# Kernel tuning notes

Measured on AMD Instinct MI355X. Metric: run time of the kernel, lower is better.

## Reference

```python
import jax, jax.numpy as jnp
import numpy as np

HID = 768        # config.hidden_size
MM_HID = 1024    # config.mmodal_hidden_size
N_Q = 64         # config.num_queries
WIN = 512        # config.window_size
LN_EPS = 1e-5


def _window_starts(m, n, w):
    # mirrors split_tensor's start-index logic (static, computed in numpy)
    step = max(1, (m - w) // (n - 1))
    starts = []
    for i in range(n):
        s = i * step
        if s + w > m:
            s = m - w
        starts.append(s)
    return np.asarray(starts, dtype=np.int32)


def layernorm(x, g, b):
    mu = jnp.mean(x, axis=-1, keepdims=True)
    var = jnp.var(x, axis=-1, keepdims=True)
    return (x - mu) * jax.lax.rsqrt(var + LN_EPS) * g + b


def setup_inputs() -> dict:
    key = jax.random.key(0)
    ks = jax.random.split(key, 12)
    b, m, li = 4, 8192, 77
    s = lambda fan_in: 1.0 / np.sqrt(fan_in)
    inp = {
        'x_mmodal': jax.random.normal(ks[0], (b, m, MM_HID), jnp.float32),
        'inst_feats': jax.random.normal(ks[1], (b, li, HID), jnp.float32),
        'queries': jax.random.normal(ks[2], (1, N_Q, HID), jnp.float32),
        'W_proj': jax.random.normal(ks[3], (HID, HID), jnp.float32) * s(HID),
        'b_proj': jnp.zeros((HID,), jnp.float32),
        'W_kv_inst': jax.random.normal(ks[4], (HID, 2 * HID), jnp.float32) * s(HID),
        'b_kv_inst': jnp.zeros((2 * HID,), jnp.float32),
        'W_out_inst': jax.random.normal(ks[5], (HID, HID), jnp.float32) * s(HID),
        'b_out_inst': jnp.zeros((HID,), jnp.float32),
        'W_kv_mm': jax.random.normal(ks[6], (MM_HID, 2 * HID), jnp.float32) * s(MM_HID),
        'b_kv_mm': jnp.zeros((2 * HID,), jnp.float32),
        'W_out_mm': jax.random.normal(ks[7], (HID, HID), jnp.float32) * s(HID),
        'b_out_mm': jnp.zeros((HID,), jnp.float32),
        'ln_g': jnp.ones((HID,), jnp.float32),
        'ln_b': jnp.zeros((HID,), jnp.float32),
    }
    return inp


def reference(x_mmodal, inst_feats, queries, W_proj, b_proj, W_kv_inst,
              b_kv_inst, W_out_inst, b_out_inst, W_kv_mm, b_kv_mm,
              W_out_mm, b_out_mm, ln_g, ln_b):
    b = x_mmodal.shape[0]
    scale = 1.0 / jnp.sqrt(jnp.asarray(HID, x_mmodal.dtype))

    # ---- dense cross-attention over instruction features ----
    inst = inst_feats @ W_proj + b_proj                      # (b, li, d)
    k, v = jnp.split(inst @ W_kv_inst + b_kv_inst, 2, axis=-1)
    k = layernorm(k, ln_g, ln_b)
    v = layernorm(v, ln_g, ln_b)
    q = jnp.broadcast_to(queries, (b, N_Q, HID))
    attn = jnp.einsum('bnd,bmd->bnm', q, k) * scale
    attn = jax.nn.softmax(attn, axis=-1)
    q = jnp.einsum('bnm,bmd->bnd', attn, v)
    q = layernorm(q @ W_out_inst + b_out_inst, ln_g, ln_b)

    # ---- swin-style overlapping windowed cross-attention over mmodal ----
    k, v = jnp.split(x_mmodal @ W_kv_mm + b_kv_mm, 2, axis=-1)
    k = layernorm(k, ln_g, ln_b)
    v = layernorm(v, ln_g, ln_b)
    m = k.shape[1]
    starts = _window_starts(m, N_Q, WIN)                     # (n,)
    idx = jnp.asarray(starts[:, None] + np.arange(WIN))      # (n, w)
    kw = k[:, idx]                                           # (b, n, w, d)
    vw = v[:, idx]                                           # (b, n, w, d)
    a = jnp.einsum('bnd,bnwd->bnw', q, kw) * scale
    a = jax.nn.softmax(a, axis=-1)
    out = jnp.einsum('bnw,bnwd->bnd', a, vw)
    out = layernorm(out @ W_out_mm + b_out_mm, ln_g, ln_b)
    return out
```

## Files before the change

### kernel.cpp

```cpp
#include <hip/hip_runtime.h>

#define HIDDEN 768
#define NQ 64
#define WINSZ 512
#define MSEQ 8192
#define BATCH 4
#define LI 77
#define MMHID 1024
#define LN_EPS 1e-5f
#define SCALE_QK 0.03608439182435161f

typedef __attribute__((ext_vector_type(8))) short short8v;
typedef __attribute__((ext_vector_type(4))) float f32x4;
typedef __attribute__((ext_vector_type(8))) unsigned short u16x8;

#define AS1 __attribute__((address_space(1)))
#define AS3 __attribute__((address_space(3)))

__device__ inline unsigned short f2bf(float f) {
    unsigned u = __float_as_uint(f);
    u += 0x7fffu + ((u >> 16) & 1u);
    return (unsigned short)(u >> 16);
}
__device__ inline float bf2f(unsigned short h) {
    return __uint_as_float(((unsigned)h) << 16);
}

__device__ inline void block_reduce2_256(float& s1, float& s2, float* sm) {
    #pragma unroll
    for (int o = 32; o; o >>= 1) { s1 += __shfl_down(s1, o); s2 += __shfl_down(s2, o); }
    int lane = threadIdx.x & 63, w = threadIdx.x >> 6;
    __syncthreads();
    if (lane == 0) { sm[w] = s1; sm[4 + w] = s2; }
    __syncthreads();
    s1 = sm[0] + sm[1] + sm[2] + sm[3];
    s2 = sm[4] + sm[5] + sm[6] + sm[7];
}

__global__ __launch_bounds__(256) void cvt_kernel(const float* __restrict__ in,
                                                  unsigned short* __restrict__ out, int n8) {
    int i = blockIdx.x * 256 + threadIdx.x;
    if (i >= n8) return;
    const float4* p = (const float4*)(in + (size_t)i * 8);
    float4 a = p[0], b = p[1];
    u16x8 o;
    o[0] = f2bf(a.x); o[1] = f2bf(a.y); o[2] = f2bf(a.z); o[3] = f2bf(a.w);
    o[4] = f2bf(b.x); o[5] = f2bf(b.y); o[6] = f2bf(b.z); o[7] = f2bf(b.w);
    *(u16x8*)(out + (size_t)i * 8) = o;
}

__global__ __launch_bounds__(256) void cvt_pad_kernel(const float* __restrict__ in,
                                                      unsigned short* __restrict__ out,
                                                      int n8_valid, int n8_total) {
    int i = blockIdx.x * 256 + threadIdx.x;
    if (i >= n8_total) return;
    u16x8 o = {};
    if (i < n8_valid) {
        const float4* p = (const float4*)(in + (size_t)i * 8);
        float4 a = p[0], b = p[1];
        o[0] = f2bf(a.x); o[1] = f2bf(a.y); o[2] = f2bf(a.z); o[3] = f2bf(a.w);
        o[4] = f2bf(b.x); o[5] = f2bf(b.y); o[6] = f2bf(b.z); o[7] = f2bf(b.w);
    }
    *(u16x8*)(out + (size_t)i * 8) = o;
}

__global__ __launch_bounds__(256) void cvt_q_kernel(const float* __restrict__ q2,
                                                    const float* __restrict__ g,
                                                    unsigned short* __restrict__ q2bf,
                                                    float* __restrict__ qgsum) {
    int blk = blockIdx.x;
    int b = blk >> 7, r = blk & 127;
    int t = threadIdx.x;
    unsigned short* orow = q2bf + (size_t)blk * HIDDEN;
    if (r >= 64) {
        orow[t] = 0; orow[t + 256] = 0; orow[t + 512] = 0;
        return;
    }
    const float* qrow = q2 + ((size_t)(b * 64 + r)) * HIDDEN;
    float v0 = qrow[t]       * g[t]       * SCALE_QK;
    float v1 = qrow[t + 256] * g[t + 256] * SCALE_QK;
    float v2 = qrow[t + 512] * g[t + 512] * SCALE_QK;
    orow[t] = f2bf(v0); orow[t + 256] = f2bf(v1); orow[t + 512] = f2bf(v2);
    float s = v0 + v1 + v2, s2 = 0.f;
    __shared__ float sm[8];
    block_reduce2_256(s, s2, sm);
    if (t == 0) qgsum[b * 64 + r] = s;
}

struct TWJobs {
    const float* W[5];
    unsigned short* Wt[5];
    int D[5];
    int C[5];
};
__global__ __launch_bounds__(256) void transW_all_kernel(TWJobs tw) {
    int z = blockIdx.z;
    int C = tw.C[z], D = tw.D[z];
    int n0 = blockIdx.x * 32, k0 = blockIdx.y * 32;
    if (n0 >= C || k0 >= D) return;
    const float* W = tw.W[z];
    unsigned short* Wt = tw.Wt[z];
    __shared__ float tile[32][33];
    int tx = threadIdx.x & 31, ty = (threadIdx.x >> 5);
    #pragma unroll
    for (int i = 0; i < 32; i += 8)
        tile[ty + i][tx] = W[(size_t)(k0 + ty + i) * C + n0 + tx];
    __syncthreads();
    #pragma unroll
    for (int i = 0; i < 32; i += 8)
        Wt[(size_t)(n0 + ty + i) * D + k0 + tx] = f2bf(tile[tx][ty + i]);
}

#define GM 32768
#define GN 1536
#define GK 1024

__global__ __launch_bounds__(256) void gemm_kv_kernel(const unsigned short* __restrict__ A,
                                                      const unsigned short* __restrict__ Bt,
                                                      const float* __restrict__ bias,
                                                      unsigned short* __restrict__ C) {
    __shared__ unsigned short sA[128 * 64];
    __shared__ unsigned short sB[128 * 64];

    int nwg = gridDim.x;
    int bid = blockIdx.x;
    int wg = bid;
    if ((nwg & 7) == 0) { int cpx = nwg >> 3; wg = (bid & 7) * cpx + (bid >> 3); }
    int bm = wg / (GN / 128), bn = wg % (GN / 128);
    int row0 = bm * 128, col0 = bn * 128;

    int tid = threadIdx.x;
    int lane = tid & 63, wid = tid >> 6;
    int wr = wid >> 1, wc = wid & 1;

    f32x4 acc[4][4] = {};

    int rS[4], cS[4];
    #pragma unroll
    for (int i = 0; i < 4; i++) {
        int ch = wid * 4 + i;
        int r = ch * 8 + (lane >> 3);
        rS[i] = r;
        cS[i] = ((lane & 7) ^ (r & 7)) << 3;
    }

    for (int k0 = 0; k0 < GK; k0 += 64) {
        #pragma unroll
        for (int i = 0; i < 4; i++) {
            int ch = wid * 4 + i;
            const unsigned short* ga = A + (size_t)(row0 + rS[i]) * GK + k0 + cS[i];
            __builtin_amdgcn_global_load_lds((const AS1 unsigned int*)ga,
                                             (AS3 unsigned int*)&sA[ch * 512], 16, 0, 0);
            const unsigned short* gb = Bt + (size_t)(col0 + rS[i]) * GK + k0 + cS[i];
            __builtin_amdgcn_global_load_lds((const AS1 unsigned int*)gb,
                                             (AS3 unsigned int*)&sB[ch * 512], 16, 0, 0);
        }
        __syncthreads();

        #pragma unroll
        for (int kk = 0; kk < 64; kk += 32) {
            int ko = (kk + ((lane >> 4) << 3)) * 2;
            short8v af[4], bf[4];
            #pragma unroll
            for (int m = 0; m < 4; m++) {
                int r = wr * 64 + m * 16 + (lane & 15);
                int addr = r * 128 + (ko ^ ((r & 7) << 4));
                af[m] = *(const short8v*)((const char*)sA + addr);
            }
            #pragma unroll
            for (int n = 0; n < 4; n++) {
                int r = wc * 64 + n * 16 + (lane & 15);
                int addr = r * 128 + (ko ^ ((r & 7) << 4));
                bf[n] = *(const short8v*)((const char*)sB + addr);
            }
            #pragma unroll
            for (int m = 0; m < 4; m++)
                #pragma unroll
                for (int n = 0; n < 4; n++)
                    acc[m][n] = __builtin_amdgcn_mfma_f32_16x16x32_bf16(af[m], bf[n], acc[m][n], 0, 0, 0);
        }
        __syncthreads();
    }

    int crow = (lane >> 4) * 4;
    int ccol = lane & 15;
    #pragma unroll
    for (int m = 0; m < 4; m++) {
        #pragma unroll
        for (int n = 0; n < 4; n++) {
            int gc = col0 + wc * 64 + n * 16 + ccol;
            float bv = bias[gc];
            #pragma unroll
            for (int j = 0; j < 4; j++) {
                int gr = row0 + wr * 64 + m * 16 + crow + j;
                C[(size_t)gr * GN + gc] = f2bf(acc[m][n][j] + bv);
            }
        }
    }
}

__global__ __launch_bounds__(256) void stats_kernel(const unsigned short* __restrict__ kv,
                                                    float2* __restrict__ stats) {
    int rh = blockIdx.x;
    const unsigned short* p = kv + (size_t)rh * 768;
    int t = threadIdx.x;
    float x0 = bf2f(p[t]), x1 = bf2f(p[t + 256]), x2 = bf2f(p[t + 512]);
    float s = x0 + x1 + x2, s2 = x0 * x0 + x1 * x1 + x2 * x2;
    __shared__ float sm[8];
    block_reduce2_256(s, s2, sm);
    if (t == 0) {
        float mu = s * (1.f / 768.f);
        float var = s2 * (1.f / 768.f) - mu * mu;
        float inv = rsqrtf(var + LN_EPS);
        stats[rh] = make_float2(mu * inv, inv);
    }
}

template <int TK, bool OUT_BF16>
__global__ __launch_bounds__(256) void gemm_tile_kernel(const unsigned short* __restrict__ A,
                                                        const unsigned short* __restrict__ Bt,
                                                        const float* __restrict__ bias,
                                                        void* __restrict__ Cout, int N) {
    __shared__ unsigned short sA[128 * 64];
    __shared__ unsigned short sB[128 * 64];

    int row0 = blockIdx.x * 128, col0 = blockIdx.y * 128;
    int tid = threadIdx.x;
    int lane = tid & 63, wid = tid >> 6;
    int wr = wid >> 1, wc = wid & 1;

    f32x4 acc[4][4] = {};

    int rS[4], cS[4];
    #pragma unroll
    for (int i = 0; i < 4; i++) {
        int ch = wid * 4 + i;
        int r = ch * 8 + (lane >> 3);
        rS[i] = r;
        cS[i] = ((lane & 7) ^ (r & 7)) << 3;
    }

    for (int k0 = 0; k0 < TK; k0 += 64) {
        #pragma unroll
        for (int i = 0; i < 4; i++) {
            int ch = wid * 4 + i;
            const unsigned short* ga = A + (size_t)(row0 + rS[i]) * TK + k0 + cS[i];
            __builtin_amdgcn_global_load_lds((const AS1 unsigned int*)ga,
                                             (AS3 unsigned int*)&sA[ch * 512], 16, 0, 0);
            const unsigned short* gb = Bt + (size_t)(col0 + rS[i]) * TK + k0 + cS[i];
            __builtin_amdgcn_global_load_lds((const AS1 unsigned int*)gb,
                                             (AS3 unsigned int*)&sB[ch * 512], 16, 0, 0);
        }
        __syncthreads();

        #pragma unroll
        for (int kk = 0; kk < 64; kk += 32) {
            int ko = (kk + ((lane >> 4) << 3)) * 2;
            short8v af[4], bf[4];
            #pragma unroll
            for (int m = 0; m < 4; m++) {
                int r = wr * 64 + m * 16 + (lane & 15);
                int addr = r * 128 + (ko ^ ((r & 7) << 4));
                af[m] = *(const short8v*)((const char*)sA + addr);
            }
            #pragma unroll
            for (int n = 0; n < 4; n++) {
                int r = wc * 64 + n * 16 + (lane & 15);
                int addr = r * 128 + (ko ^ ((r & 7) << 4));
                bf[n] = *(const short8v*)((const char*)sB + addr);
            }
            #pragma unroll
            for (int m = 0; m < 4; m++)
                #pragma unroll
                for (int n = 0; n < 4; n++)
                    acc[m][n] = __builtin_amdgcn_mfma_f32_16x16x32_bf16(af[m], bf[n], acc[m][n], 0, 0, 0);
        }
        __syncthreads();
    }

    int crow = (lane >> 4) * 4;
    int ccol = lane & 15;
    #pragma unroll
    for (int m = 0; m < 4; m++) {
        #pragma unroll
        for (int n = 0; n < 4; n++) {
            int gc = col0 + wc * 64 + n * 16 + ccol;
            float bv = bias[gc];
            #pragma unroll
            for (int j = 0; j < 4; j++) {
                int gr = row0 + wr * 64 + m * 16 + crow + j;
                float v = acc[m][n][j] + bv;
                if (OUT_BF16) ((unsigned short*)Cout)[(size_t)gr * N + gc] = f2bf(v);
                else          ((float*)Cout)[(size_t)gr * N + gc] = v;
            }
        }
    }
}

__global__ __launch_bounds__(256) void gemm_scores_kernel(const unsigned short* __restrict__ Aall,
                                                          const unsigned short* __restrict__ kv,
                                                          float* __restrict__ scores) {
    __shared__ unsigned short sA[128 * 64];
    __shared__ unsigned short sB[128 * 64];

    int b = blockIdx.y;
    int col0 = blockIdx.x * 128;
    const unsigned short* A = Aall + (size_t)b * 128 * HIDDEN;
    const unsigned short* Bt = kv + (size_t)b * MSEQ * 1536;

    int tid = threadIdx.x;
    int lane = tid & 63, wid = tid >> 6;
    int wr = wid >> 1, wc = wid & 1;

    f32x4 acc[4][4] = {};

    int rS[4], cS[4];
    #pragma unroll
    for (int i = 0; i < 4; i++) {
        int ch = wid * 4 + i;
        int r = ch * 8 + (lane >> 3);
        rS[i] = r;
        cS[i] = ((lane & 7) ^ (r & 7)) << 3;
    }

    for (int k0 = 0; k0 < HIDDEN; k0 += 64) {
        #pragma unroll
        for (int i = 0; i < 4; i++) {
            int ch = wid * 4 + i;
            const unsigned short* ga = A + (size_t)rS[i] * HIDDEN + k0 + cS[i];
            __builtin_amdgcn_global_load_lds((const AS1 unsigned int*)ga,
                                             (AS3 unsigned int*)&sA[ch * 512], 16, 0, 0);
            const unsigned short* gb = Bt + (size_t)(col0 + rS[i]) * 1536 + k0 + cS[i];
            __builtin_amdgcn_global_load_lds((const AS1 unsigned int*)gb,
                                             (AS3 unsigned int*)&sB[ch * 512], 16, 0, 0);
        }
        __syncthreads();

        #pragma unroll
        for (int kk = 0; kk < 64; kk += 32) {
            int ko = (kk + ((lane >> 4) << 3)) * 2;
            short8v af[4], bf[4];
            #pragma unroll
            for (int m = 0; m < 4; m++) {
                int r = wr * 64 + m * 16 + (lane & 15);
                int addr = r * 128 + (ko ^ ((r & 7) << 4));
                af[m] = *(const short8v*)((const char*)sA + addr);
            }
            #pragma unroll
            for (int n = 0; n < 4; n++) {
                int r = wc * 64 + n * 16 + (lane & 15);
                int addr = r * 128 + (ko ^ ((r & 7) << 4));
                bf[n] = *(const short8v*)((const char*)sB + addr);
            }
            #pragma unroll
            for (int m = 0; m < 4; m++)
                #pragma unroll
                for (int n = 0; n < 4; n++)
                    acc[m][n] = __builtin_amdgcn_mfma_f32_16x16x32_bf16(af[m], bf[n], acc[m][n], 0, 0, 0);
        }
        __syncthreads();
    }

    int crow = (lane >> 4) * 4;
    int ccol = lane & 15;
    #pragma unroll
    for (int m = 0; m < 4; m++) {
        #pragma unroll
        for (int n = 0; n < 4; n++) {
            int gc = col0 + wc * 64 + n * 16 + ccol;
            #pragma unroll
            for (int j = 0; j < 4; j++) {
                int gr = wr * 64 + m * 16 + crow + j;
                if (gr < 64)
                    scores[((size_t)(b * 64 + gr)) * MSEQ + gc] = acc[m][n][j];
            }
        }
    }
}

__global__ __launch_bounds__(512) void win_softmax_kernel(const float* __restrict__ scores,
                                                          const float2* __restrict__ stats,
                                                          const float* __restrict__ qgsum,
                                                          unsigned short* __restrict__ P_abs,
                                                          float* __restrict__ s2out) {
    int bidx = blockIdx.x;
    int b = bidx >> 6, n = bidx & 63;
    int step = (MSEQ - WINSZ) / (NQ - 1);
    int s = n * step;
    if (s + WINSZ > MSEQ) s = MSEQ - WINSZ;

    __shared__ float sm[8];
    int t = threadIdx.x, lane = t & 63, w = t >> 6;
    int r_abs = s + t;
    size_t rowidx = (size_t)b * MSEQ + r_abs;
    float2 stk = stats[rowidx * 2 + 0];
    float qg = qgsum[b * 64 + n];
    float a = stk.y * scores[((size_t)(b * 64 + n)) * MSEQ + r_abs] - qg * stk.x;

    float m = a;
    #pragma unroll
    for (int o = 32; o; o >>= 1) m = fmaxf(m, __shfl_down(m, o));
    if (lane == 0) sm[w] = m;
    __syncthreads();
    m = sm[0];
    #pragma unroll
    for (int i = 1; i < 8; i++) m = fmaxf(m, sm[i]);
    float e = expf(a - m);
    float ssum = e;
    #pragma unroll
    for (int o = 32; o; o >>= 1) ssum += __shfl_down(ssum, o);
    __syncthreads();
    if (lane == 0) sm[w] = ssum;
    __syncthreads();
    ssum = 0;
    #pragma unroll
    for (int i = 0; i < 8; i++) ssum += sm[i];
    float p = e / ssum;

    float2 stv = stats[rowidx * 2 + 1];
    float pt = p * stv.y;
    float s2p = p * stv.x;
    #pragma unroll
    for (int o = 32; o; o >>= 1) s2p += __shfl_down(s2p, o);
    __syncthreads();
    if (lane == 0) sm[w] = s2p;
    __syncthreads();
    if (t == 0) {
        float s2 = 0;
        #pragma unroll
        for (int i = 0; i < 8; i++) s2 += sm[i];
        s2out[b * 64 + n] = s2;
    }

    unsigned short* prow = P_abs + ((size_t)(b * 64 + n)) * MSEQ;
    for (int pos = t; pos < MSEQ; pos += 512)
        if (pos < s || pos >= s + WINSZ) prow[pos] = 0;
    prow[r_abs] = f2bf(pt);
}

__global__ __launch_bounds__(768) void pv_chunk_kernel(const unsigned short* __restrict__ P_abs,
                                                       const unsigned short* __restrict__ kv,
                                                       float* __restrict__ out_acc) {
    int b = blockIdx.y;
    int r0 = blockIdx.x * 64;
    int t = threadIdx.x;

    int n_lo = (r0 >= 512) ? ((r0 - 512) / 121 + 1) : 0;
    int n_hi = (r0 + 63) / 121;
    if (n_hi > 63) n_hi = 63;

    __shared__ float pw[5][64];
    if (t < 5 * 64) {
        int ni = t >> 6, r = t & 63;
        int n = n_lo + ni;
        float v = 0.f;
        if (n <= n_hi)
            v = bf2f(P_abs[((size_t)(b * 64 + n)) * MSEQ + r0 + r]);
        pw[ni][r] = v;
    }
    __syncthreads();

    const unsigned short* vbase = kv + ((size_t)(b * MSEQ + r0)) * 1536 + 768;
    float acc[5] = {};
    #pragma unroll 8
    for (int r = 0; r < 64; ++r) {
        float v = bf2f(vbase[(size_t)r * 1536 + t]);
        #pragma unroll
        for (int ni = 0; ni < 5; ni++) acc[ni] = fmaf(v, pw[ni][r], acc[ni]);
    }
    #pragma unroll
    for (int ni = 0; ni < 5; ni++) {
        int n = n_lo + ni;
        if (n <= n_hi)
            atomicAdd(&out_acc[((size_t)(b * 64 + n)) * HIDDEN + t], acc[ni]);
    }
}

__global__ __launch_bounds__(256) void out_affine_kernel(const float* __restrict__ o_acc,
                                                         const float* __restrict__ s2,
                                                         const float* __restrict__ g,
                                                         const float* __restrict__ bb,
                                                         unsigned short* __restrict__ a_bf) {
    int i = blockIdx.x * 256 + threadIdx.x;
    if (i >= BATCH * NQ * HIDDEN) return;
    int n = i / HIDDEN, d = i - n * HIDDEN;
    a_bf[i] = f2bf(g[d] * (o_acc[i] - s2[n]) + bb[d]);
}

__global__ __launch_bounds__(256) void ln_f32_rows(float* __restrict__ base,
                                                   const float* __restrict__ g,
                                                   const float* __restrict__ b) {
    int rh = blockIdx.x;
    float* p = base + (size_t)rh * 768;
    int t = threadIdx.x;
    float x0 = p[t], x1 = p[t + 256], x2 = p[t + 512];
    float s = x0 + x1 + x2, s2 = x0 * x0 + x1 * x1 + x2 * x2;
    __shared__ float sm[8];
    block_reduce2_256(s, s2, sm);
    float mu = s * (1.f / 768.f);
    float var = s2 * (1.f / 768.f) - mu * mu;
    float inv = rsqrtf(var + LN_EPS);
    p[t]       = (x0 - mu) * inv * g[t]       + b[t];
    p[t + 256] = (x1 - mu) * inv * g[t + 256] + b[t + 256];
    p[t + 512] = (x2 - mu) * inv * g[t + 512] + b[t + 512];
}

__global__ __launch_bounds__(256) void attn_inst_kernel(const float* __restrict__ queries,
                                                        const float* __restrict__ kv,
                                                        unsigned short* __restrict__ qatt) {
    int bidx = blockIdx.x;
    int b = bidx >> 6, n = bidx & 63;
    __shared__ float qs[HIDDEN];
    __shared__ float sc[LI], sc2[LI];
    int t = threadIdx.x, lane = t & 63, w = t >> 6;
    const float* q = queries + (size_t)n * HIDDEN;
    for (int d = t; d < HIDDEN; d += 256) qs[d] = q[d];
    __syncthreads();
    const float* kb = kv + (size_t)b * LI * 1536;
    for (int j = w; j < LI; j += 4) {
        const float* kr = kb + (size_t)j * 1536;
        float a = 0;
        #pragma unroll
        for (int i = 0; i < 12; i++) { int d = lane + i * 64; a = fmaf(kr[d], qs[d], a); }
        #pragma unroll
        for (int o = 32; o; o >>= 1) a += __shfl_down(a, o);
        if (lane == 0) sc[j] = a * SCALE_QK;
    }
    __syncthreads();
    float m = -1e30f;
    for (int j = 0; j < LI; j++) m = fmaxf(m, sc[j]);
    if (t < LI) sc2[t] = expf(sc[t] - m);
    __syncthreads();
    float s = 0;
    for (int j = 0; j < LI; j++) s += sc2[j];
    float inv = 1.f / s;
    float o0 = 0, o1 = 0, o2 = 0;
    for (int j = 0; j < LI; j++) {
        float p = sc2[j] * inv;
        const float* vr = kb + (size_t)j * 1536 + 768;
        o0 = fmaf(p, vr[t], o0);
        o1 = fmaf(p, vr[t + 256], o1);
        o2 = fmaf(p, vr[t + 512], o2);
    }
    unsigned short* orow = qatt + ((size_t)b * NQ + n) * HIDDEN;
    orow[t] = f2bf(o0); orow[t + 256] = f2bf(o1); orow[t + 512] = f2bf(o2);
}

extern "C" void kernel_launch(void* const* d_in, const int* in_sizes, int n_in,
                              void* d_out, int out_size, void* d_ws, size_t ws_size,
                              hipStream_t stream) {
    (void)in_sizes; (void)n_in; (void)out_size; (void)ws_size;
    const float* x_mm    = (const float*)d_in[0];
    const float* instf   = (const float*)d_in[1];
    const float* queries = (const float*)d_in[2];
    const float* W_proj  = (const float*)d_in[3];
    const float* b_proj  = (const float*)d_in[4];
    const float* W_kvi   = (const float*)d_in[5];
    const float* b_kvi   = (const float*)d_in[6];
    const float* W_oi    = (const float*)d_in[7];
    const float* b_oi    = (const float*)d_in[8];
    const float* W_kvm   = (const float*)d_in[9];
    const float* b_kvm   = (const float*)d_in[10];
    const float* W_om    = (const float*)d_in[11];
    const float* b_om    = (const float*)d_in[12];
    const float* ln_g    = (const float*)d_in[13];
    const float* ln_b    = (const float*)d_in[14];
    float* out = (float*)d_out;

    char* ws = (char*)d_ws;
    size_t off = 0;
    auto carve = [&](size_t bytes) -> char* {
        char* p = ws + off;
        off += (bytes + 255) & ~(size_t)255;
        return p;
    };
    unsigned short* x_bf   = (unsigned short*)carve((size_t)BATCH * MSEQ * MMHID * 2);
    unsigned short* wtm_bf = (unsigned short*)carve((size_t)2 * HIDDEN * MMHID * 2);
    unsigned short* kv_mm  = (unsigned short*)carve((size_t)BATCH * MSEQ * 2 * HIDDEN * 2);
    unsigned short* wp_bf  = (unsigned short*)carve((size_t)768 * 768 * 2);
    unsigned short* wkvi_bf= (unsigned short*)carve((size_t)1536 * 768 * 2);
    unsigned short* woi_bf = (unsigned short*)carve((size_t)768 * 768 * 2);
    unsigned short* wom_bf = (unsigned short*)carve((size_t)768 * 768 * 2);
    unsigned short* a1_bf  = (unsigned short*)carve((size_t)384 * 768 * 2);
    unsigned short* inst_bf= (unsigned short*)carve((size_t)384 * 768 * 2);
    float*          kv_inst= (float*)carve((size_t)384 * 1536 * 4);
    unsigned short* qatt_bf= (unsigned short*)carve((size_t)256 * 768 * 2);
    float*          q2     = (float*)carve((size_t)256 * 768 * 4);
    unsigned short* q2bf   = (unsigned short*)carve((size_t)BATCH * 128 * 768 * 2);
    float*          scores = (float*)carve((size_t)BATCH * 64 * MSEQ * 4);
    unsigned short* P_abs  = (unsigned short*)carve((size_t)BATCH * 64 * MSEQ * 2);
    float*          o_acc  = (float*)carve((size_t)BATCH * 64 * 768 * 4);
    unsigned short* a_bf   = (unsigned short*)carve((size_t)256 * 768 * 2);
    float2*         stats  = (float2*)carve((size_t)BATCH * MSEQ * 2 * sizeof(float2));
    float*          qgsum  = (float*)carve((size_t)256 * 4);
    float*          s2     = (float*)carve((size_t)256 * 4);

    TWJobs tw;
    tw.W[0] = W_kvm;  tw.Wt[0] = wtm_bf;  tw.D[0] = 1024; tw.C[0] = 1536;
    tw.W[1] = W_proj; tw.Wt[1] = wp_bf;   tw.D[1] = 768;  tw.C[1] = 768;
    tw.W[2] = W_kvi;  tw.Wt[2] = wkvi_bf; tw.D[2] = 768;  tw.C[2] = 1536;
    tw.W[3] = W_oi;   tw.Wt[3] = woi_bf;  tw.D[3] = 768;  tw.C[3] = 768;
    tw.W[4] = W_om;   tw.Wt[4] = wom_bf;  tw.D[4] = 768;  tw.C[4] = 768;
    transW_all_kernel<<<dim3(48, 32, 5), 256, 0, stream>>>(tw);

    int n8 = BATCH * MSEQ * MMHID / 8;
    cvt_kernel<<<(n8 + 255) / 256, 256, 0, stream>>>(x_mm, x_bf, n8);
    gemm_kv_kernel<<<(GM / 128) * (GN / 128), 256, 0, stream>>>(x_bf, wtm_bf, b_kvm, kv_mm);
    stats_kernel<<<BATCH * MSEQ * 2, 256, 0, stream>>>(kv_mm, stats);

    cvt_pad_kernel<<<(384 * 768 / 8 + 255) / 256, 256, 0, stream>>>(instf, a1_bf,
                                                                    BATCH * LI * 768 / 8, 384 * 768 / 8);
    gemm_tile_kernel<768, true><<<dim3(3, 6), 256, 0, stream>>>(a1_bf, wp_bf, b_proj, inst_bf, 768);
    gemm_tile_kernel<768, false><<<dim3(3, 12), 256, 0, stream>>>(inst_bf, wkvi_bf, b_kvi, kv_inst, 1536);
    ln_f32_rows<<<BATCH * LI * 2, 256, 0, stream>>>(kv_inst, ln_g, ln_b);
    attn_inst_kernel<<<BATCH * NQ, 256, 0, stream>>>(queries, kv_inst, qatt_bf);
    gemm_tile_kernel<768, false><<<dim3(2, 6), 256, 0, stream>>>(qatt_bf, woi_bf, b_oi, q2, 768);
    ln_f32_rows<<<BATCH * NQ, 256, 0, stream>>>(q2, ln_g, ln_b);

    hipMemsetAsync(o_acc, 0, (size_t)BATCH * 64 * 768 * 4, stream);
    cvt_q_kernel<<<BATCH * 128, 256, 0, stream>>>(q2, ln_g, q2bf, qgsum);
    gemm_scores_kernel<<<dim3(MSEQ / 128, BATCH), 256, 0, stream>>>(q2bf, kv_mm, scores);
    win_softmax_kernel<<<BATCH * NQ, 512, 0, stream>>>(scores, stats, qgsum, P_abs, s2);
    pv_chunk_kernel<<<dim3(MSEQ / 64, BATCH), 768, 0, stream>>>(P_abs, kv_mm, o_acc);
    out_affine_kernel<<<(BATCH * NQ * HIDDEN + 255) / 256, 256, 0, stream>>>(o_acc, s2, ln_g, ln_b, a_bf);

    gemm_tile_kernel<768, false><<<dim3(2, 6), 256, 0, stream>>>(a_bf, wom_bf, b_om, out, 768);
    ln_f32_rows<<<BATCH * NQ, 256, 0, stream>>>(out, ln_g, ln_b);
}
```

Before: 350.2 us.

## Fuse fp32-to-bf16 conversion and LayerNorm stats into the KV GEMM

The KV projection GEMM now reads fp32 x_mmodal directly, converts it to bf16 in registers and writes it into swizzled LDS. This removes the separate conversion pass and its intermediate bf16 buffer. The GEMM epilogue also accumulates per-row sum and sum-of-squares for each K/V half with shuffle reductions and atomics, and a small finalize kernel replaces the stats kernel that re-read the whole KV output. In exchange, the A tile is now loaded synchronously through registers and twice the A bytes are re-read across column tiles. Atomic traffic and a memset are also added.

After: 566.2 us. 61.7% more time.

```diff
diff --git a/kernel.cpp b/kernel.cpp
--- a/kernel.cpp
+++ b/kernel.cpp
@@ -35,18 +35,6 @@
     __syncthreads();
     s1 = sm[0] + sm[1] + sm[2] + sm[3];
     s2 = sm[4] + sm[5] + sm[6] + sm[7];
-}
-
-__global__ __launch_bounds__(256) void cvt_kernel(const float* __restrict__ in,
-                                                  unsigned short* __restrict__ out, int n8) {
-    int i = blockIdx.x * 256 + threadIdx.x;
-    if (i >= n8) return;
-    const float4* p = (const float4*)(in + (size_t)i * 8);
-    float4 a = p[0], b = p[1];
-    u16x8 o;
-    o[0] = f2bf(a.x); o[1] = f2bf(a.y); o[2] = f2bf(a.z); o[3] = f2bf(a.w);
-    o[4] = f2bf(b.x); o[5] = f2bf(b.y); o[6] = f2bf(b.z); o[7] = f2bf(b.w);
-    *(u16x8*)(out + (size_t)i * 8) = o;
 }
 
 __global__ __launch_bounds__(256) void cvt_pad_kernel(const float* __restrict__ in,
@@ -115,10 +103,11 @@
 #define GN 1536
 #define GK 1024
 
-__global__ __launch_bounds__(256) void gemm_kv_kernel(const unsigned short* __restrict__ A,
+__global__ __launch_bounds__(256) void gemm_kv_kernel(const float* __restrict__ Af,
                                                       const unsigned short* __restrict__ Bt,
                                                       const float* __restrict__ bias,
-                                                      unsigned short* __restrict__ C) {
+                                                      unsigned short* __restrict__ C,
+                                                      float2* __restrict__ stats_acc) {
     __shared__ unsigned short sA[128 * 64];
     __shared__ unsigned short sB[128 * 64];
 
@@ -144,16 +133,39 @@
         cS[i] = ((lane & 7) ^ (r & 7)) << 3;
     }
 
+    int rA[4], c8A[4], dstA[4];
+    #pragma unroll
+    for (int u = 0; u < 4; u++) {
+        int idx = u * 2048 + tid * 8;
+        int r = idx >> 6;
+        int c8 = (idx >> 3) & 7;
+        rA[u] = r; c8A[u] = c8;
+        dstA[u] = r * 128 + ((c8 ^ (r & 7)) << 4);
+    }
+
     for (int k0 = 0; k0 < GK; k0 += 64) {
         #pragma unroll
         for (int i = 0; i < 4; i++) {
             int ch = wid * 4 + i;
-            const unsigned short* ga = A + (size_t)(row0 + rS[i]) * GK + k0 + cS[i];
-            __builtin_amdgcn_global_load_lds((const AS1 unsigned int*)ga,
-                                             (AS3 unsigned int*)&sA[ch * 512], 16, 0, 0);
             const unsigned short* gb = Bt + (size_t)(col0 + rS[i]) * GK + k0 + cS[i];
             __builtin_amdgcn_global_load_lds((const AS1 unsigned int*)gb,
                                              (AS3 unsigned int*)&sB[ch * 512], 16, 0, 0);
+        }
+        float4 fa[4][2];
+        #pragma unroll
+        for (int u = 0; u < 4; u++) {
+            const float* ga = Af + (size_t)(row0 + rA[u]) * GK + k0 + c8A[u] * 8;
+            fa[u][0] = *(const float4*)ga;
+            fa[u][1] = *(const float4*)(ga + 4);
+        }
+        #pragma unroll
+        for (int u = 0; u < 4; u++) {
+            u16x8 h;
+            h[0] = f2bf(fa[u][0].x); h[1] = f2bf(fa[u][0].y);
+            h[2] = f2bf(fa[u][0].z); h[3] = f2bf(fa[u][0].w);
+            h[4] = f2bf(fa[u][1].x); h[5] = f2bf(fa[u][1].y);
+            h[6] = f2bf(fa[u][1].z); h[7] = f2bf(fa[u][1].w);
+            *(u16x8*)((char*)sA + dstA[u]) = h;
         }
         __syncthreads();
 
@@ -184,8 +196,10 @@
 
     int crow = (lane >> 4) * 4;
     int ccol = lane & 15;
+    int half = (col0 >= 768) ? 1 : 0;
     #pragma unroll
     for (int m = 0; m < 4; m++) {
+        float rs[4] = {}, rq[4] = {};
         #pragma unroll
         for (int n = 0; n < 4; n++) {
             int gc = col0 + wc * 64 + n * 16 + ccol;
@@ -193,27 +207,34 @@
             #pragma unroll
             for (int j = 0; j < 4; j++) {
                 int gr = row0 + wr * 64 + m * 16 + crow + j;
-                C[(size_t)gr * GN + gc] = f2bf(acc[m][n][j] + bv);
-            }
-        }
-    }
-}
-
-__global__ __launch_bounds__(256) void stats_kernel(const unsigned short* __restrict__ kv,
-                                                    float2* __restrict__ stats) {
-    int rh = blockIdx.x;
-    const unsigned short* p = kv + (size_t)rh * 768;
-    int t = threadIdx.x;
-    float x0 = bf2f(p[t]), x1 = bf2f(p[t + 256]), x2 = bf2f(p[t + 512]);
-    float s = x0 + x1 + x2, s2 = x0 * x0 + x1 * x1 + x2 * x2;
-    __shared__ float sm[8];
-    block_reduce2_256(s, s2, sm);
-    if (t == 0) {
-        float mu = s * (1.f / 768.f);
-        float var = s2 * (1.f / 768.f) - mu * mu;
-        float inv = rsqrtf(var + LN_EPS);
-        stats[rh] = make_float2(mu * inv, inv);
-    }
+                float v = acc[m][n][j] + bv;
+                C[(size_t)gr * GN + gc] = f2bf(v);
+                rs[j] += v; rq[j] += v * v;
+            }
+        }
+        #pragma unroll
+        for (int j = 0; j < 4; j++) {
+            float s = rs[j], q = rq[j];
+            #pragma unroll
+            for (int o = 8; o; o >>= 1) { s += __shfl_xor(s, o); q += __shfl_xor(q, o); }
+            if (ccol == 0) {
+                int gr = row0 + wr * 64 + m * 16 + crow + j;
+                atomicAdd(&stats_acc[(size_t)gr * 2 + half].x, s);
+                atomicAdd(&stats_acc[(size_t)gr * 2 + half].y, q);
+            }
+        }
+    }
+}
+
+__global__ __launch_bounds__(256) void stats_fin_kernel(const float2* __restrict__ accum,
+                                                        float2* __restrict__ stats, int n) {
+    int i = blockIdx.x * 256 + threadIdx.x;
+    if (i >= n) return;
+    float2 a = accum[i];
+    float mu = a.x * (1.f / 768.f);
+    float var = a.y * (1.f / 768.f) - mu * mu;
+    float inv = rsqrtf(var + LN_EPS);
+    stats[i] = make_float2(mu * inv, inv);
 }
 
 template <int TK, bool OUT_BF16>
@@ -574,7 +595,6 @@
         off += (bytes + 255) & ~(size_t)255;
         return p;
     };
-    unsigned short* x_bf   = (unsigned short*)carve((size_t)BATCH * MSEQ * MMHID * 2);
     unsigned short* wtm_bf = (unsigned short*)carve((size_t)2 * HIDDEN * MMHID * 2);
     unsigned short* kv_mm  = (unsigned short*)carve((size_t)BATCH * MSEQ * 2 * HIDDEN * 2);
     unsigned short* wp_bf  = (unsigned short*)carve((size_t)768 * 768 * 2);
@@ -591,6 +611,7 @@
     unsigned short* P_abs  = (unsigned short*)carve((size_t)BATCH * 64 * MSEQ * 2);
     float*          o_acc  = (float*)carve((size_t)BATCH * 64 * 768 * 4);
     unsigned short* a_bf   = (unsigned short*)carve((size_t)256 * 768 * 2);
+    float2*         stat_s = (float2*)carve((size_t)BATCH * MSEQ * 2 * sizeof(float2));
     float2*         stats  = (float2*)carve((size_t)BATCH * MSEQ * 2 * sizeof(float2));
     float*          qgsum  = (float*)carve((size_t)256 * 4);
     float*          s2     = (float*)carve((size_t)256 * 4);
@@ -603,10 +624,9 @@
     tw.W[4] = W_om;   tw.Wt[4] = wom_bf;  tw.D[4] = 768;  tw.C[4] = 768;
     transW_all_kernel<<<dim3(48, 32, 5), 256, 0, stream>>>(tw);
 
-    int n8 = BATCH * MSEQ * MMHID / 8;
-    cvt_kernel<<<(n8 + 255) / 256, 256, 0, stream>>>(x_mm, x_bf, n8);
-    gemm_kv_kernel<<<(GM / 128) * (GN / 128), 256, 0, stream>>>(x_bf, wtm_bf, b_kvm, kv_mm);
-    stats_kernel<<<BATCH * MSEQ * 2, 256, 0, stream>>>(kv_mm, stats);
+    hipMemsetAsync(stat_s, 0, (size_t)BATCH * MSEQ * 2 * sizeof(float2), stream);
+    gemm_kv_kernel<<<(GM / 128) * (GN / 128), 256, 0, stream>>>(x_mm, wtm_bf, b_kvm, kv_mm, stat_s);
+    stats_fin_kernel<<<(BATCH * MSEQ * 2 + 255) / 256, 256, 0, stream>>>(stat_s, stats, BATCH * MSEQ * 2);
 
     cvt_pad_kernel<<<(384 * 768 / 8 + 255) / 256, 256, 0, stream>>>(instf, a1_bf,
                                                                     BATCH * LI * 768 / 8, 384 * 768 / 8);
```

## Fuse fp32-to-bf16 conversion of x_mmodal into KV GEMM A-tile loading

Applied to the files above, without the earlier changes.

Drops the standalone conversion kernel that wrote a bf16 copy of the large x_mmodal tensor. The KV GEMM now reads fp32 A directly into registers, converts to bf16 and stores into swizzled LDS, prefetching the next K-slice into registers double-buffered across steps. This removes a full write and re-read of the 64MB bf16 intermediate. In exchange each GEMM tile, 12 column tiles per row block, re-reads A as fp32 at twice the bytes, and register pressure rises.

Measured after the change: 503.4 us. 43.7% more time.

```diff
diff --git a/kernel.cpp b/kernel.cpp
--- a/kernel.cpp
+++ b/kernel.cpp
@@ -35,18 +35,6 @@
     __syncthreads();
     s1 = sm[0] + sm[1] + sm[2] + sm[3];
     s2 = sm[4] + sm[5] + sm[6] + sm[7];
-}
-
-__global__ __launch_bounds__(256) void cvt_kernel(const float* __restrict__ in,
-                                                  unsigned short* __restrict__ out, int n8) {
-    int i = blockIdx.x * 256 + threadIdx.x;
-    if (i >= n8) return;
-    const float4* p = (const float4*)(in + (size_t)i * 8);
-    float4 a = p[0], b = p[1];
-    u16x8 o;
-    o[0] = f2bf(a.x); o[1] = f2bf(a.y); o[2] = f2bf(a.z); o[3] = f2bf(a.w);
-    o[4] = f2bf(b.x); o[5] = f2bf(b.y); o[6] = f2bf(b.z); o[7] = f2bf(b.w);
-    *(u16x8*)(out + (size_t)i * 8) = o;
 }
 
 __global__ __launch_bounds__(256) void cvt_pad_kernel(const float* __restrict__ in,
@@ -115,7 +103,7 @@
 #define GN 1536
 #define GK 1024
 
-__global__ __launch_bounds__(256) void gemm_kv_kernel(const unsigned short* __restrict__ A,
+__global__ __launch_bounds__(256) void gemm_kv_kernel(const float* __restrict__ Af,
                                                       const unsigned short* __restrict__ Bt,
                                                       const float* __restrict__ bias,
                                                       unsigned short* __restrict__ C) {
@@ -144,19 +132,51 @@
         cS[i] = ((lane & 7) ^ (r & 7)) << 3;
     }
 
-    for (int k0 = 0; k0 < GK; k0 += 64) {
+    int rA[4], c8A[4], dstA[4];
+    #pragma unroll
+    for (int u = 0; u < 4; u++) {
+        int idx = u * 2048 + tid * 8;
+        int r = idx >> 6;
+        int c8 = (idx >> 3) & 7;
+        rA[u] = r; c8A[u] = c8;
+        dstA[u] = r * 128 + ((c8 ^ (r & 7)) << 4);
+    }
+
+    float4 fa[4][2], fb[4][2];
+    #pragma unroll
+    for (int u = 0; u < 4; u++) {
+        const float* ga = Af + (size_t)(row0 + rA[u]) * GK + c8A[u] * 8;
+        fa[u][0] = *(const float4*)ga;
+        fa[u][1] = *(const float4*)(ga + 4);
+    }
+
+    auto STEP = [&](int k0, float4 (&cur)[4][2], float4 (&nxt)[4][2]) {
         #pragma unroll
         for (int i = 0; i < 4; i++) {
             int ch = wid * 4 + i;
-            const unsigned short* ga = A + (size_t)(row0 + rS[i]) * GK + k0 + cS[i];
-            __builtin_amdgcn_global_load_lds((const AS1 unsigned int*)ga,
-                                             (AS3 unsigned int*)&sA[ch * 512], 16, 0, 0);
             const unsigned short* gb = Bt + (size_t)(col0 + rS[i]) * GK + k0 + cS[i];
             __builtin_amdgcn_global_load_lds((const AS1 unsigned int*)gb,
                                              (AS3 unsigned int*)&sB[ch * 512], 16, 0, 0);
         }
+        #pragma unroll
+        for (int u = 0; u < 4; u++) {
+            u16x8 h;
+            h[0] = f2bf(cur[u][0].x); h[1] = f2bf(cur[u][0].y);
+            h[2] = f2bf(cur[u][0].z); h[3] = f2bf(cur[u][0].w);
+            h[4] = f2bf(cur[u][1].x); h[5] = f2bf(cur[u][1].y);
+            h[6] = f2bf(cur[u][1].z); h[7] = f2bf(cur[u][1].w);
+            *(u16x8*)((char*)sA + dstA[u]) = h;
+        }
         __syncthreads();
-
+        int k1 = k0 + 64;
+        if (k1 < GK) {
+            #pragma unroll
+            for (int u = 0; u < 4; u++) {
+                const float* ga = Af + (size_t)(row0 + rA[u]) * GK + k1 + c8A[u] * 8;
+                nxt[u][0] = *(const float4*)ga;
+                nxt[u][1] = *(const float4*)(ga + 4);
+            }
+        }
         #pragma unroll
         for (int kk = 0; kk < 64; kk += 32) {
             int ko = (kk + ((lane >> 4) << 3)) * 2;
@@ -180,6 +200,11 @@
                     acc[m][n] = __builtin_amdgcn_mfma_f32_16x16x32_bf16(af[m], bf[n], acc[m][n], 0, 0, 0);
         }
         __syncthreads();
+    };
+
+    for (int k0 = 0; k0 < GK; k0 += 128) {
+        STEP(k0, fa, fb);
+        STEP(k0 + 64, fb, fa);
     }
 
     int crow = (lane >> 4) * 4;
@@ -574,7 +599,6 @@
         off += (bytes + 255) & ~(size_t)255;
         return p;
     };
-    unsigned short* x_bf   = (unsigned short*)carve((size_t)BATCH * MSEQ * MMHID * 2);
     unsigned short* wtm_bf = (unsigned short*)carve((size_t)2 * HIDDEN * MMHID * 2);
     unsigned short* kv_mm  = (unsigned short*)carve((size_t)BATCH * MSEQ * 2 * HIDDEN * 2);
     unsigned short* wp_bf  = (unsigned short*)carve((size_t)768 * 768 * 2);
@@ -603,9 +627,7 @@
     tw.W[4] = W_om;   tw.Wt[4] = wom_bf;  tw.D[4] = 768;  tw.C[4] = 768;
     transW_all_kernel<<<dim3(48, 32, 5), 256, 0, stream>>>(tw);
 
-    int n8 = BATCH * MSEQ * MMHID / 8;
-    cvt_kernel<<<(n8 + 255) / 256, 256, 0, stream>>>(x_mm, x_bf, n8);
-    gemm_kv_kernel<<<(GM / 128) * (GN / 128), 256, 0, stream>>>(x_bf, wtm_bf, b_kvm, kv_mm);
+    gemm_kv_kernel<<<(GM / 128) * (GN / 128), 256, 0, stream>>>(x_mm, wtm_bf, b_kvm, kv_mm);
     stats_kernel<<<BATCH * MSEQ * 2, 256, 0, stream>>>(kv_mm, stats);
 
     cvt_pad_kernel<<<(384 * 768 / 8 + 255) / 256, 256, 0, stream>>>(instf, a1_bf,
```
